# Kernel tuning notes

Measured on AMD Instinct MI355X. Metric: run time of the kernel, lower is better.

The kernel has to match this reference:

```python
import jax, jax.numpy as jnp
import numpy as np

B, N, DIN, DOUT = 8, 2048, 512, 512

def setup_inputs() -> dict:
    key = jax.random.key(0)
    kx, ka, kw, kb, kattn = jax.random.split(key, 5)
    x = jax.random.normal(kx, (B, N, DIN), dtype=jnp.float32)
    adjacency_matrix = jax.random.randint(ka, (B, N, N), 0, 2, dtype=jnp.int32)
    # nn.Linear(in,out): weight [out,in], bias [out]
    lim_w = float(np.sqrt(1.0 / DIN))
    W = jax.random.uniform(kw, (DOUT, DIN), minval=-lim_w, maxval=lim_w, dtype=jnp.float32)
    b = jax.random.uniform(kb, (DOUT,), minval=-lim_w, maxval=lim_w, dtype=jnp.float32)
    # xavier_uniform for attn [out,out]
    lim_a = float(np.sqrt(6.0 / (DOUT + DOUT)))
    attn = jax.random.uniform(kattn, (DOUT, DOUT), minval=-lim_a, maxval=lim_a, dtype=jnp.float32)
    return {"x": x, "adjacency_matrix": adjacency_matrix, "W": W, "b": b, "attn": attn}

def reference(x, adjacency_matrix, W, b, attn):
    h = jnp.einsum('bni,oi->bno', x, W) + b                 # [B,N,DOUT]
    ha = jnp.einsum('bmi,ij->bmj', h, attn)                  # h @ attn
    scores = jnp.einsum('bmj,bnj->bmn', ha, h)               # bilinear pairwise scores
    scores = jnp.where(adjacency_matrix == 0, -jnp.inf, scores)
    attn_weights = jax.nn.softmax(scores, axis=-1)           # adjacency-masked softmax
    x_out = jnp.einsum('bmn,bnd->bmd', attn_weights, h)      # weighted aggregation
    return jax.nn.elu(x_out)
```

## Files before the change

### kernel.cpp

```cpp
#include <hip/hip_runtime.h>
#include <cstdint>
#include <cstddef>

typedef unsigned short u16;
using f16x8 = __attribute__((ext_vector_type(8))) _Float16;
using f32x4 = __attribute__((ext_vector_type(4))) float;
using u16x4 = __attribute__((ext_vector_type(4))) unsigned short;

__device__ __forceinline__ u16 f2h(float f) {
  union { _Float16 h; u16 u; } c;
  c.h = (_Float16)f;
  return c.u;
}

__device__ __forceinline__ void gl_lds16(const void* g, void* lds) {
  __builtin_amdgcn_global_load_lds(
      (const __attribute__((address_space(1))) void*)(uintptr_t)g,
      (__attribute__((address_space(3))) void*)(uint32_t)(uintptr_t)lds,
      16, 0, 0);
}

template <int MODE>
__global__ __launch_bounds__(256) void gemm_bt(
    const u16* __restrict__ A, const u16* __restrict__ Bt,
    void* __restrict__ Cv, const float* __restrict__ bias,
    int M, int Ncols, int K,
    long long strideA, long long strideB, long long strideC)
{
  __shared__ __align__(16) u16 sA[128 * 32];
  __shared__ __align__(16) u16 sB[128 * 32];

  const int bz = blockIdx.z;
  A  += (size_t)bz * strideA;
  Bt += (size_t)bz * strideB;

  const int m0 = blockIdx.y * 128;
  const int n0 = blockIdx.x * 128;
  const int t    = threadIdx.x;
  const int lane = t & 63;
  const int wave = t >> 6;
  const int wm   = (wave >> 1) * 64;
  const int wn   = (wave & 1) * 64;
  const int lm   = lane & 15;
  const int quad = lane >> 4;

  f32x4 acc[4][4];
#pragma unroll
  for (int i = 0; i < 4; ++i)
#pragma unroll
    for (int j = 0; j < 4; ++j) acc[i][j] = f32x4{0.f, 0.f, 0.f, 0.f};

  const int r0 = t >> 2,        c0 = t & 3;
  const int r1 = (t + 256) >> 2, c1 = t & 3;
  const int ldsb0 = (t & ~63) * 8;
  const int ldsb1 = ((t & ~63) + 256) * 8;

  const int nk = K >> 5;
  for (int kc = 0; kc < nk; ++kc) {
    const int kb = kc * 32;
    gl_lds16(A  + (size_t)(m0 + r0) * K + kb + c0 * 8, sA + ldsb0);
    gl_lds16(A  + (size_t)(m0 + r1) * K + kb + c1 * 8, sA + ldsb1);
    gl_lds16(Bt + (size_t)(n0 + r0) * K + kb + c0 * 8, sB + ldsb0);
    gl_lds16(Bt + (size_t)(n0 + r1) * K + kb + c1 * 8, sB + ldsb1);
    __syncthreads();

    f16x8 af[4], bf[4];
#pragma unroll
    for (int i = 0; i < 4; ++i) {
      af[i] = *(const f16x8*)(sA + (wm + i * 16 + lm) * 32 + quad * 8);
      bf[i] = *(const f16x8*)(sB + (wn + i * 16 + lm) * 32 + quad * 8);
    }
#pragma unroll
    for (int i = 0; i < 4; ++i)
#pragma unroll
      for (int j = 0; j < 4; ++j)
        acc[i][j] = __builtin_amdgcn_mfma_f32_16x16x32_f16(af[i], bf[j], acc[i][j], 0, 0, 0);
    __syncthreads();
  }

  if (MODE == 0) {
    u16* C = (u16*)Cv + (size_t)bz * strideC;
#pragma unroll
    for (int j = 0; j < 4; ++j) {
      const int col = n0 + wn + j * 16 + lm;
      const float bv = bias ? bias[col] : 0.f;
#pragma unroll
      for (int i = 0; i < 4; ++i)
#pragma unroll
        for (int r = 0; r < 4; ++r) {
          const int row = m0 + wm + i * 16 + quad * 4 + r;
          C[(size_t)row * Ncols + col] = f2h(acc[i][j][r] + bv);
        }
    }
  } else {
    float* C = (float*)Cv + (size_t)bz * strideC;
#pragma unroll
    for (int j = 0; j < 4; ++j) {
      const int col = n0 + wn + j * 16 + lm;
#pragma unroll
      for (int i = 0; i < 4; ++i)
#pragma unroll
        for (int r = 0; r < 4; ++r) {
          const int row = m0 + wm + i * 16 + quad * 4 + r;
          float v = acc[i][j][r];
          if (MODE == 2) v = v > 0.f ? v : expm1f(v);
          C[(size_t)row * Ncols + col] = v;
        }
    }
  }
}

__global__ __launch_bounds__(256) void masked_softmax(
    const float* __restrict__ S, const int* __restrict__ adj, u16* __restrict__ P)
{
  const size_t row = blockIdx.x;
  const float* s = S + row * 2048;
  const int*   a = adj + row * 2048;
  u16*         p = P + row * 2048;
  const int t = threadIdx.x;

  float v[8];
#pragma unroll
  for (int i = 0; i < 2; ++i) {
    float4 sv = ((const float4*)s)[t + i * 256];
    int4   av = ((const int4*)a)[t + i * 256];
    v[i * 4 + 0] = av.x ? sv.x : -1e30f;
    v[i * 4 + 1] = av.y ? sv.y : -1e30f;
    v[i * 4 + 2] = av.z ? sv.z : -1e30f;
    v[i * 4 + 3] = av.w ? sv.w : -1e30f;
  }
  float mx = v[0];
#pragma unroll
  for (int i = 1; i < 8; ++i) mx = fmaxf(mx, v[i]);
#pragma unroll
  for (int o = 32; o > 0; o >>= 1) mx = fmaxf(mx, __shfl_xor(mx, o));
  __shared__ float red[4];
  if ((t & 63) == 0) red[t >> 6] = mx;
  __syncthreads();
  mx = fmaxf(fmaxf(red[0], red[1]), fmaxf(red[2], red[3]));
  __syncthreads();

  float e[8]; float sum = 0.f;
#pragma unroll
  for (int i = 0; i < 8; ++i) { e[i] = __expf(v[i] - mx); sum += e[i]; }
#pragma unroll
  for (int o = 32; o > 0; o >>= 1) sum += __shfl_xor(sum, o);
  if ((t & 63) == 0) red[t >> 6] = sum;
  __syncthreads();
  sum = red[0] + red[1] + red[2] + red[3];
  const float inv = 1.f / sum;

#pragma unroll
  for (int i = 0; i < 2; ++i) {
    u16x4 o4;
    o4[0] = f2h(e[i * 4 + 0] * inv);
    o4[1] = f2h(e[i * 4 + 1] * inv);
    o4[2] = f2h(e[i * 4 + 2] * inv);
    o4[3] = f2h(e[i * 4 + 3] * inv);
    ((u16x4*)p)[t + i * 256] = o4;
  }
}

__global__ __launch_bounds__(256) void transpose_u16(
    const u16* __restrict__ in, u16* __restrict__ outp, int R, int C)
{
  __shared__ u16 tile[64][65];
  const size_t base = (size_t)blockIdx.z * R * C;
  const int r0 = blockIdx.y * 64, c0 = blockIdx.x * 64;
  const int t = threadIdx.x;
  const int c = t & 63, rr = t >> 6;
#pragma unroll
  for (int i = 0; i < 16; ++i) {
    const int r = rr + i * 4;
    tile[r][c] = in[base + (size_t)(r0 + r) * C + c0 + c];
  }
  __syncthreads();
  const int rp = t & 63, cc = t >> 6;
#pragma unroll
  for (int i = 0; i < 16; ++i) {
    const int cq = cc + i * 4;
    outp[base + (size_t)(c0 + cq) * R + r0 + rp] = tile[rp][cq];
  }
}

__global__ __launch_bounds__(256) void cvt_f32_f16(
    const float* __restrict__ in, u16* __restrict__ outp, int n4)
{
  const int i = blockIdx.x * 256 + threadIdx.x;
  if (i >= n4) return;
  float4 v = ((const float4*)in)[i];
  u16x4 o; o[0] = f2h(v.x); o[1] = f2h(v.y); o[2] = f2h(v.z); o[3] = f2h(v.w);
  ((u16x4*)outp)[i] = o;
}

__global__ __launch_bounds__(256) void transpose_cvt(
    const float* __restrict__ in, u16* __restrict__ outp, int R, int C)
{
  const int idx = blockIdx.x * 256 + threadIdx.x;
  const int i = idx / C, j = idx % C;
  outp[(size_t)j * R + i] = f2h(in[idx]);
}

extern "C" void kernel_launch(void* const* d_in, const int* in_sizes, int n_in,
                              void* d_out, int out_size, void* d_ws, size_t ws_size,
                              hipStream_t stream) {
  (void)in_sizes; (void)n_in; (void)out_size;
  const float* x    = (const float*)d_in[0];
  const int*   adj  = (const int*)d_in[1];
  const float* W    = (const float*)d_in[2];
  const float* bvec = (const float*)d_in[3];
  const float* attn = (const float*)d_in[4];
  float* out = (float*)d_out;

  constexpr int B = 8, N = 2048, D = 512;
  constexpr size_t MN = (size_t)B * N;

  char* ws = (char*)d_ws;
  size_t off = 0;
  auto take = [&](size_t bytes) -> char* {
    char* p = ws + off;
    off += (bytes + 255) & ~(size_t)255;
    return p;
  };
  u16* xh   = (u16*)take(MN * D * 2);
  u16* Wh   = (u16*)take((size_t)D * D * 2);
  u16* attT = (u16*)take((size_t)D * D * 2);
  u16* h    = (u16*)take(MN * D * 2);
  u16* hT   = (u16*)take(MN * D * 2);
  u16* ha   = (u16*)take(MN * D * 2);

  auto al = [](size_t b) { return (b + 255) & ~(size_t)255; };
  const size_t szSf = al((size_t)B * N * N * 4), szPf = al((size_t)B * N * N * 2);
  const size_t szSb = al((size_t)N * N * 4),     szPb = al((size_t)N * N * 2);
  const bool full  = ws_size >= off + szSf + szPf;
  const bool ok_pb = ws_size >= off + szSb + szPb;
  if (!full && !ok_pb) return;

  cvt_f32_f16<<<dim3((unsigned)(MN * D / 4 / 256)), 256, 0, stream>>>(x, xh, (int)(MN * D / 4));
  cvt_f32_f16<<<dim3(D * D / 4 / 256), 256, 0, stream>>>(W, Wh, D * D / 4);
  transpose_cvt<<<dim3(D * D / 256), 256, 0, stream>>>(attn, attT, D, D);

  gemm_bt<0><<<dim3(D / 128, MN / 128, 1), 256, 0, stream>>>(
      xh, Wh, h, bvec, (int)MN, D, D, 0, 0, 0);
  transpose_u16<<<dim3(D / 64, N / 64, B), 256, 0, stream>>>(h, hT, N, D);
  gemm_bt<0><<<dim3(D / 128, MN / 128, 1), 256, 0, stream>>>(
      h, attT, ha, nullptr, (int)MN, D, D, 0, 0, 0);

  if (full) {
    float* S = (float*)take(szSf);
    u16*   P = (u16*)take(szPf);
    gemm_bt<1><<<dim3(N / 128, N / 128, B), 256, 0, stream>>>(
        ha, h, S, nullptr, N, N, D,
        (long long)N * D, (long long)N * D, (long long)N * N);
    masked_softmax<<<dim3((unsigned)(B * N)), 256, 0, stream>>>(S, adj, P);
    gemm_bt<2><<<dim3(D / 128, N / 128, B), 256, 0, stream>>>(
        P, hT, out, nullptr, N, D, N,
        (long long)N * N, (long long)D * N, (long long)N * D);
  } else {
    float* S = (float*)take(szSb);
    u16*   P = (u16*)take(szPb);
    for (int b = 0; b < B; ++b) {
      gemm_bt<1><<<dim3(N / 128, N / 128, 1), 256, 0, stream>>>(
          ha + (size_t)b * N * D, h + (size_t)b * N * D, S, nullptr, N, N, D, 0, 0, 0);
      masked_softmax<<<dim3(N), 256, 0, stream>>>(S, adj + (size_t)b * N * N, P);
      gemm_bt<2><<<dim3(D / 128, N / 128, 1), 256, 0, stream>>>(
          P, hT + (size_t)b * D * N, out + (size_t)b * N * D, nullptr, N, D, N, 0, 0, 0);
    }
  }
}
```

Baseline: 440.4 us.

## Fuse score GEMM, masked softmax and aggregation into flash-style kernel with bit-packed adjacency

Replaces the three-stage path (fp32 score GEMM into a B*N*N buffer, masked softmax writing fp16 P, then P@h GEMM) with one flash-attention style kernel. It computes score tiles in registers, applies an online softmax with running max and sum, and accumulates P@V. The adjacency matrix is packed into 16-bit masks by a new kernel, so the main loop reads far fewer bytes. This removes the large intermediate S and P traffic. The cost is only 256 blocks, V fragments loaded straight from global memory with no LDS staging, and many barriers per tile.

After: 508.7 us. +15.5%, slower.

```diff
diff --git a/kernel.cpp b/kernel.cpp
--- a/kernel.cpp
+++ b/kernel.cpp
@@ -78,87 +78,205 @@
     __syncthreads();
   }
 
-  if (MODE == 0) {
-    u16* C = (u16*)Cv + (size_t)bz * strideC;
-#pragma unroll
-    for (int j = 0; j < 4; ++j) {
-      const int col = n0 + wn + j * 16 + lm;
-      const float bv = bias ? bias[col] : 0.f;
+  u16* C = (u16*)Cv + (size_t)bz * strideC;
+#pragma unroll
+  for (int j = 0; j < 4; ++j) {
+    const int col = n0 + wn + j * 16 + lm;
+    const float bv = bias ? bias[col] : 0.f;
+#pragma unroll
+    for (int i = 0; i < 4; ++i)
+#pragma unroll
+      for (int r = 0; r < 4; ++r) {
+        const int row = m0 + wm + i * 16 + quad * 4 + r;
+        C[(size_t)row * Ncols + col] = f2h(acc[i][j][r] + bv);
+      }
+  }
+}
+
+__global__ __launch_bounds__(512, 2) void flash_gat(
+    const u16* __restrict__ haP, const u16* __restrict__ hP,
+    const u16* __restrict__ hTP, const u16* __restrict__ adjb,
+    float* __restrict__ outP)
+{
+  __shared__ __align__(16) u16 sQ[2 * 64 * 32];
+  __shared__ __align__(16) u16 sK[2 * 128 * 32];
+  __shared__ __align__(16) u16 sP[64 * 136];
+  __shared__ float rmA[4][64];
+  __shared__ float rsA[4][64];
+  __shared__ float m_sh[64], l_sh[64], al_sh[64];
+
+  const int t     = threadIdx.x;
+  const int batch = blockIdx.x & 7;
+  const int q0    = (blockIdx.x >> 3) << 6;
+  const int lane  = t & 63;
+  const int wave  = t >> 6;
+  const int lm    = lane & 15;
+  const int quad  = lane >> 4;
+  const int wm    = (wave >> 2) * 32;
+  const int wn    = (wave & 3) * 32;
+  const int wd    = wave * 64;
+
+  const u16* Q  = haP + ((size_t)batch * 2048 + q0) * 512;
+  const u16* K  = hP  + (size_t)batch * 2048 * 512;
+  const u16* V  = hTP + (size_t)batch * 512 * 2048;
+  const u16* Ar = adjb + ((size_t)batch * 2048 + q0) * 128;
+  float* Co = outP + ((size_t)batch * 2048 + q0) * 512;
+
+  if (t < 64) { m_sh[t] = -1e30f; l_sh[t] = 0.f; }
+
+  f32x4 o[4][4];
+#pragma unroll
+  for (int i = 0; i < 4; ++i)
+#pragma unroll
+    for (int j = 0; j < 4; ++j) o[i][j] = f32x4{0.f, 0.f, 0.f, 0.f};
+
+  const int kkq = t >> 8, rowq = (t >> 2) & 63, chq = t & 3;
+  const u16* qsrc = Q + rowq * 512 + kkq * 32 + chq * 8;
+  u16* qdst  = sQ + (t & ~63) * 8;
+  const int rowk = t >> 2, chk = t & 3;
+  u16* kdst0 = sK + (t & ~63) * 8;
+  u16* kdst1 = sK + ((t & ~63) + 512) * 8;
+
+  for (int nt = 0; nt < 16; ++nt) {
+    const int n0 = nt * 128;
+    f32x4 sacc[2][2];
+#pragma unroll
+    for (int i = 0; i < 2; ++i)
+#pragma unroll
+      for (int j = 0; j < 2; ++j) sacc[i][j] = f32x4{0.f, 0.f, 0.f, 0.f};
+
+    const u16* Krow = K + (size_t)(n0 + rowk) * 512 + chk * 8;
+    for (int kc = 0; kc < 8; ++kc) {
+      const int kb = kc * 64;
+      gl_lds16(qsrc + kb, qdst);
+      gl_lds16(Krow + kb, kdst0);
+      gl_lds16(Krow + kb + 32, kdst1);
+      __syncthreads();
+#pragma unroll
+      for (int kk = 0; kk < 2; ++kk) {
+        f16x8 aq[2], bk[2];
+#pragma unroll
+        for (int i = 0; i < 2; ++i)
+          aq[i] = *(const f16x8*)(sQ + kk * 2048 + (wm + i * 16 + lm) * 32 + quad * 8);
+#pragma unroll
+        for (int j = 0; j < 2; ++j)
+          bk[j] = *(const f16x8*)(sK + kk * 4096 + (wn + j * 16 + lm) * 32 + quad * 8);
+#pragma unroll
+        for (int i = 0; i < 2; ++i)
+#pragma unroll
+          for (int j = 0; j < 2; ++j)
+            sacc[i][j] = __builtin_amdgcn_mfma_f32_16x16x32_f16(aq[i], bk[j], sacc[i][j], 0, 0, 0);
+      }
+      __syncthreads();
+    }
+
+#pragma unroll
+    for (int i = 0; i < 2; ++i)
+#pragma unroll
+      for (int r = 0; r < 4; ++r) {
+        const int R = wm + i * 16 + quad * 4 + r;
+        const u16* ab = Ar + R * 128 + nt * 8 + (wn >> 4);
+        const unsigned w0 = ab[0], w1 = ab[1];
+        float s0 = sacc[i][0][r], s1 = sacc[i][1][r];
+        s0 = ((w0 >> lm) & 1u) ? s0 : -1e30f;
+        s1 = ((w1 >> lm) & 1u) ? s1 : -1e30f;
+        sacc[i][0][r] = s0; sacc[i][1][r] = s1;
+        float m = fmaxf(s0, s1);
+        m = fmaxf(m, __shfl_xor(m, 1));
+        m = fmaxf(m, __shfl_xor(m, 2));
+        m = fmaxf(m, __shfl_xor(m, 4));
+        m = fmaxf(m, __shfl_xor(m, 8));
+        if (lm == 0) rmA[wave & 3][R] = m;
+      }
+    __syncthreads();
+
+#pragma unroll
+    for (int i = 0; i < 2; ++i)
+#pragma unroll
+      for (int r = 0; r < 4; ++r) {
+        const int R = wm + i * 16 + quad * 4 + r;
+        const float cm = fmaxf(fmaxf(rmA[0][R], rmA[1][R]), fmaxf(rmA[2][R], rmA[3][R]));
+        const float nm = fmaxf(m_sh[R], cm);
+        const float p0 = __expf(sacc[i][0][r] - nm);
+        const float p1 = __expf(sacc[i][1][r] - nm);
+        sP[R * 136 + wn + lm]      = f2h(p0);
+        sP[R * 136 + wn + 16 + lm] = f2h(p1);
+        float rr = p0 + p1;
+        rr += __shfl_xor(rr, 1);
+        rr += __shfl_xor(rr, 2);
+        rr += __shfl_xor(rr, 4);
+        rr += __shfl_xor(rr, 8);
+        if (lm == 0) rsA[wave & 3][R] = rr;
+      }
+    __syncthreads();
+
+    if (t < 64) {
+      const float cm = fmaxf(fmaxf(rmA[0][t], rmA[1][t]), fmaxf(rmA[2][t], rmA[3][t]));
+      const float mo = m_sh[t];
+      const float nm = fmaxf(mo, cm);
+      const float a  = __expf(mo - nm);
+      l_sh[t]  = a * l_sh[t] + rsA[0][t] + rsA[1][t] + rsA[2][t] + rsA[3][t];
+      m_sh[t]  = nm;
+      al_sh[t] = a;
+    }
+    __syncthreads();
+
+#pragma unroll
+    for (int i = 0; i < 4; ++i)
+#pragma unroll
+      for (int r = 0; r < 4; ++r) {
+        const float a = al_sh[i * 16 + quad * 4 + r];
+#pragma unroll
+        for (int j = 0; j < 4; ++j) o[i][j][r] *= a;
+      }
+#pragma unroll
+    for (int kb = 0; kb < 4; ++kb) {
+      f16x8 ap[4], bv[4];
 #pragma unroll
       for (int i = 0; i < 4; ++i)
-#pragma unroll
-        for (int r = 0; r < 4; ++r) {
-          const int row = m0 + wm + i * 16 + quad * 4 + r;
-          C[(size_t)row * Ncols + col] = f2h(acc[i][j][r] + bv);
-        }
-    }
-  } else {
-    float* C = (float*)Cv + (size_t)bz * strideC;
-#pragma unroll
-    for (int j = 0; j < 4; ++j) {
-      const int col = n0 + wn + j * 16 + lm;
+        ap[i] = *(const f16x8*)(sP + (i * 16 + lm) * 136 + kb * 32 + quad * 8);
+#pragma unroll
+      for (int j = 0; j < 4; ++j)
+        bv[j] = *(const f16x8*)(V + (size_t)(wd + j * 16 + lm) * 2048 + n0 + kb * 32 + quad * 8);
 #pragma unroll
       for (int i = 0; i < 4; ++i)
 #pragma unroll
-        for (int r = 0; r < 4; ++r) {
-          const int row = m0 + wm + i * 16 + quad * 4 + r;
-          float v = acc[i][j][r];
-          if (MODE == 2) v = v > 0.f ? v : expm1f(v);
-          C[(size_t)row * Ncols + col] = v;
-        }
-    }
-  }
-}
-
-__global__ __launch_bounds__(256) void masked_softmax(
-    const float* __restrict__ S, const int* __restrict__ adj, u16* __restrict__ P)
-{
-  const size_t row = blockIdx.x;
-  const float* s = S + row * 2048;
-  const int*   a = adj + row * 2048;
-  u16*         p = P + row * 2048;
-  const int t = threadIdx.x;
-
-  float v[8];
-#pragma unroll
-  for (int i = 0; i < 2; ++i) {
-    float4 sv = ((const float4*)s)[t + i * 256];
-    int4   av = ((const int4*)a)[t + i * 256];
-    v[i * 4 + 0] = av.x ? sv.x : -1e30f;
-    v[i * 4 + 1] = av.y ? sv.y : -1e30f;
-    v[i * 4 + 2] = av.z ? sv.z : -1e30f;
-    v[i * 4 + 3] = av.w ? sv.w : -1e30f;
-  }
-  float mx = v[0];
-#pragma unroll
-  for (int i = 1; i < 8; ++i) mx = fmaxf(mx, v[i]);
-#pragma unroll
-  for (int o = 32; o > 0; o >>= 1) mx = fmaxf(mx, __shfl_xor(mx, o));
-  __shared__ float red[4];
-  if ((t & 63) == 0) red[t >> 6] = mx;
-  __syncthreads();
-  mx = fmaxf(fmaxf(red[0], red[1]), fmaxf(red[2], red[3]));
-  __syncthreads();
-
-  float e[8]; float sum = 0.f;
-#pragma unroll
-  for (int i = 0; i < 8; ++i) { e[i] = __expf(v[i] - mx); sum += e[i]; }
-#pragma unroll
-  for (int o = 32; o > 0; o >>= 1) sum += __shfl_xor(sum, o);
-  if ((t & 63) == 0) red[t >> 6] = sum;
-  __syncthreads();
-  sum = red[0] + red[1] + red[2] + red[3];
-  const float inv = 1.f / sum;
-
-#pragma unroll
-  for (int i = 0; i < 2; ++i) {
-    u16x4 o4;
-    o4[0] = f2h(e[i * 4 + 0] * inv);
-    o4[1] = f2h(e[i * 4 + 1] * inv);
-    o4[2] = f2h(e[i * 4 + 2] * inv);
-    o4[3] = f2h(e[i * 4 + 3] * inv);
-    ((u16x4*)p)[t + i * 256] = o4;
-  }
+        for (int j = 0; j < 4; ++j)
+          o[i][j] = __builtin_amdgcn_mfma_f32_16x16x32_f16(ap[i], bv[j], o[i][j], 0, 0, 0);
+    }
+  }
+
+#pragma unroll
+  for (int i = 0; i < 4; ++i)
+#pragma unroll
+    for (int r = 0; r < 4; ++r) {
+      const int R = i * 16 + quad * 4 + r;
+      const float inv = 1.f / l_sh[R];
+#pragma unroll
+      for (int j = 0; j < 4; ++j) {
+        float v = o[i][j][r] * inv;
+        v = v > 0.f ? v : expm1f(v);
+        Co[(size_t)R * 512 + wd + j * 16 + lm] = v;
+      }
+    }
+}
+
+__global__ __launch_bounds__(256) void adj_pack(
+    const int* __restrict__ adj, u16* __restrict__ outw, int nwords)
+{
+  const int i = blockIdx.x * 256 + threadIdx.x;
+  if (i >= nwords) return;
+  const int4* p = (const int4*)(adj + (size_t)i * 16);
+  unsigned w = 0;
+#pragma unroll
+  for (int k = 0; k < 4; ++k) {
+    int4 v = p[k];
+    w |= (unsigned)(v.x != 0) << (k * 4 + 0);
+    w |= (unsigned)(v.y != 0) << (k * 4 + 1);
+    w |= (unsigned)(v.z != 0) << (k * 4 + 2);
+    w |= (unsigned)(v.w != 0) << (k * 4 + 3);
+  }
+  outw[i] = (u16)w;
 }
 
 __global__ __launch_bounds__(256) void transpose_u16(
@@ -228,17 +346,14 @@
   u16* h    = (u16*)take(MN * D * 2);
   u16* hT   = (u16*)take(MN * D * 2);
   u16* ha   = (u16*)take(MN * D * 2);
-
-  auto al = [](size_t b) { return (b + 255) & ~(size_t)255; };
-  const size_t szSf = al((size_t)B * N * N * 4), szPf = al((size_t)B * N * N * 2);
-  const size_t szSb = al((size_t)N * N * 4),     szPb = al((size_t)N * N * 2);
-  const bool full  = ws_size >= off + szSf + szPf;
-  const bool ok_pb = ws_size >= off + szSb + szPb;
-  if (!full && !ok_pb) return;
+  u16* adjb = (u16*)take((size_t)B * N * (N / 16) * 2);
+  if (off > ws_size) return;
 
   cvt_f32_f16<<<dim3((unsigned)(MN * D / 4 / 256)), 256, 0, stream>>>(x, xh, (int)(MN * D / 4));
   cvt_f32_f16<<<dim3(D * D / 4 / 256), 256, 0, stream>>>(W, Wh, D * D / 4);
   transpose_cvt<<<dim3(D * D / 256), 256, 0, stream>>>(attn, attT, D, D);
+  const int nwords = (int)(MN * (N / 16));
+  adj_pack<<<dim3(nwords / 256), 256, 0, stream>>>(adj, adjb, nwords);
 
   gemm_bt<0><<<dim3(D / 128, MN / 128, 1), 256, 0, stream>>>(
       xh, Wh, h, bvec, (int)MN, D, D, 0, 0, 0);
@@ -246,25 +361,5 @@
   gemm_bt<0><<<dim3(D / 128, MN / 128, 1), 256, 0, stream>>>(
       h, attT, ha, nullptr, (int)MN, D, D, 0, 0, 0);
 
-  if (full) {
-    float* S = (float*)take(szSf);
-    u16*   P = (u16*)take(szPf);
-    gemm_bt<1><<<dim3(N / 128, N / 128, B), 256, 0, stream>>>(
-        ha, h, S, nullptr, N, N, D,
-        (long long)N * D, (long long)N * D, (long long)N * N);
-    masked_softmax<<<dim3((unsigned)(B * N)), 256, 0, stream>>>(S, adj, P);
-    gemm_bt<2><<<dim3(D / 128, N / 128, B), 256, 0, stream>>>(
-        P, hT, out, nullptr, N, D, N,
-        (long long)N * N, (long long)D * N, (long long)N * D);
-  } else {
-    float* S = (float*)take(szSb);
-    u16*   P = (u16*)take(szPb);
-    for (int b = 0; b < B; ++b) {
-      gemm_bt<1><<<dim3(N / 128, N / 128, 1), 256, 0, stream>>>(
-          ha + (size_t)b * N * D, h + (size_t)b * N * D, S, nullptr, N, N, D, 0, 0, 0);
-      masked_softmax<<<dim3(N), 256, 0, stream>>>(S, adj + (size_t)b * N * N, P);
-      gemm_bt<2><<<dim3(D / 128, N / 128, 1), 256, 0, stream>>>(
-          P, hT + (size_t)b * D * N, out + (size_t)b * N * D, nullptr, N, D, N, 0, 0, 0);
-    }
-  }
-}
+  flash_gat<<<dim3(256), 512, 0, stream>>>(ha, h, hT, adjb, out);
+}
```
